# Performance work log

Measured on AMD Instinct MI355X. Metric: run time of the kernel, lower is better.

The kernel has to match this reference:

```python
import jax, jax.numpy as jnp
import numpy as np

N_NODES = 100000
N_EDGES = 1600000
D = 32  # atom and bond feature dim


def _mlp(x, W1, b1, W2, b2, W3, b3):
    # fff: Linear(in,128) -> ReLU -> Linear(128,64) -> ReLU -> Linear(64,32)
    h = jax.nn.relu(x @ W1 + b1)
    h = jax.nn.relu(h @ W2 + b2)
    return h @ W3 + b3


def _init_mlp(key, in_dim):
    ks = jax.random.split(key, 3)
    def lin(k, fan_in, fan_out):
        bound = 1.0 / np.sqrt(fan_in)
        kw, kb = jax.random.split(k)
        W = jax.random.uniform(kw, (fan_in, fan_out), jnp.float32, -bound, bound)
        b = jax.random.uniform(kb, (fan_out,), jnp.float32, -bound, bound)
        return W, b
    W1, b1 = lin(ks[0], in_dim, 128)
    W2, b2 = lin(ks[1], 128, 64)
    W3, b3 = lin(ks[2], 64, 32)
    return W1, b1, W2, b2, W3, b3


def setup_inputs() -> dict:
    key = jax.random.key(0)
    k_bonds, k_a1, k_a2, k_atoms, k_e, k_v = jax.random.split(key, 6)
    inp = {
        "bonds": jax.random.normal(k_bonds, (N_EDGES, D), jnp.float32),
        "bond_atom_1": jax.random.randint(k_a1, (N_EDGES,), 0, N_NODES, jnp.int64),
        "bond_atom_2": jax.random.randint(k_a2, (N_EDGES,), 0, N_NODES, jnp.int64),
        "atoms": jax.random.normal(k_atoms, (N_NODES, D), jnp.float32),
    }
    We1, be1, We2, be2, We3, be3 = _init_mlp(k_e, 96)
    Wv1, bv1, Wv2, bv2, Wv3, bv3 = _init_mlp(k_v, 64)
    inp.update(We1=We1, be1=be1, We2=We2, be2=be2, We3=We3, be3=be3,
               Wv1=Wv1, bv1=bv1, Wv2=Wv2, bv2=bv2, Wv3=Wv3, bv3=bv3)
    return inp


def reference(bonds, bond_atom_1, bond_atom_2, atoms,
              We1, be1, We2, be2, We3, be3,
              Wv1, bv1, Wv2, bv2, Wv3, bv3):
    # Edge update: gather endpoint atom features, concat with bond feats, MLP
    atom1 = atoms[bond_atom_1]                    # [E, D]
    atom2 = atoms[bond_atom_2]                    # [E, D]
    e_in = jnp.concatenate([atom1, atom2, bonds], axis=1)  # [E, 3D]
    new_bonds = _mlp(e_in, We1, be1, We2, be2, We3, be3)    # [E, 32]

    # Node update: scatter-mean new bond features onto target atoms
    # (PyG default flow aggregates messages at edge_index[1] == bond_atom_2)
    n = atoms.shape[0]
    seg_sum = jax.ops.segment_sum(new_bonds, bond_atom_2, num_segments=n)
    counts = jax.ops.segment_sum(jnp.ones((new_bonds.shape[0],), new_bonds.dtype),
                                 bond_atom_2, num_segments=n)
    mean_bonds = seg_sum / jnp.maximum(counts, 1.0)[:, None]  # [N, 32]

    v_in = jnp.concatenate([mean_bonds, atoms], axis=1)        # [N, 64]
    new_atoms = _mlp(v_in, Wv1, bv1, Wv2, bv2, Wv3, bv3)       # [N, 32]
    return (new_atoms, new_bonds)
```

## Files before the change

### kernel.cpp

```cpp
#include <hip/hip_runtime.h>
#include <hip/hip_bf16.h>

#define NN 100000
#define NE 1600000
#define NB_SCAN 391

typedef __attribute__((ext_vector_type(8))) short bfrag8;
typedef __attribute__((ext_vector_type(4))) float f32x4;
typedef __attribute__((ext_vector_type(4))) unsigned short us4;
typedef __attribute__((ext_vector_type(8))) unsigned short us8;

__device__ __forceinline__ unsigned short f2bf(float f) {
  unsigned int u = __float_as_uint(f);
  u += 0x7fffu + ((u >> 16) & 1u);
  return (unsigned short)(u >> 16);
}

__device__ __forceinline__ f32x4 mfma16(bfrag8 a, bfrag8 b, f32x4 c) {
  return __builtin_amdgcn_mfma_f32_16x16x32_bf16(a, b, c, 0, 0, 0);
}

__device__ __forceinline__ bfrag8 ld_cvt8(const float* p) {
  float4 a = *(const float4*)p;
  float4 b = *(const float4*)(p + 4);
  bfrag8 r;
  r[0] = (short)f2bf(a.x); r[1] = (short)f2bf(a.y);
  r[2] = (short)f2bf(a.z); r[3] = (short)f2bf(a.w);
  r[4] = (short)f2bf(b.x); r[5] = (short)f2bf(b.y);
  r[6] = (short)f2bf(b.z); r[7] = (short)f2bf(b.w);
  return r;
}

__device__ __forceinline__ void gload_lds16(const void* g, void* l) {
  __builtin_amdgcn_global_load_lds(
      (const __attribute__((address_space(1))) unsigned int*)g,
      (__attribute__((address_space(3))) unsigned int*)l, 16, 0, 0);
}

__device__ __forceinline__ void stage8(unsigned short* dst, const float* src) {
  float4 a = *(const float4*)src;
  float4 b = *(const float4*)(src + 4);
  us8 o;
  o[0] = f2bf(a.x); o[1] = f2bf(a.y); o[2] = f2bf(a.z); o[3] = f2bf(a.w);
  o[4] = f2bf(b.x); o[5] = f2bf(b.y); o[6] = f2bf(b.z); o[7] = f2bf(b.w);
  *(us8*)dst = o;
}

__global__ void pack_w(const float* __restrict__ src, unsigned short* __restrict__ dst,
                       int K, int N) {
  int i = blockIdx.x * 256 + threadIdx.x;
  if (i >= K * N) return;
  int j = i & 7;
  int gc = i >> 3;
  int c = gc % N;
  int g = gc / N;
  dst[i] = f2bf(src[(g * 8 + j) * N + c]);
}

__global__ void count_k(const int* __restrict__ a2, int* __restrict__ cnt) {
  int e = blockIdx.x * 256 + threadIdx.x;
  if (e < NE) atomicAdd(&cnt[a2[e]], 1);
}

__global__ void scan_blocks(const int* __restrict__ cnt, int* __restrict__ off,
                            int* __restrict__ bsum) {
  __shared__ int s[256];
  const int t = threadIdx.x;
  const int idx = blockIdx.x * 256 + t;
  int v = (idx < NN) ? cnt[idx] : 0;
  s[t] = v;
  __syncthreads();
  for (int d = 1; d < 256; d <<= 1) {
    int x = (t >= d) ? s[t - d] : 0;
    __syncthreads();
    s[t] += x;
    __syncthreads();
  }
  if (idx < NN) off[idx] = s[t] - v;
  if (t == 255) bsum[blockIdx.x] = s[255];
}

__global__ void scan_bsum(int* __restrict__ bsum) {
  __shared__ int s[512];
  const int t = threadIdx.x;
  int v = (t < NB_SCAN) ? bsum[t] : 0;
  s[t] = v;
  __syncthreads();
  for (int d = 1; d < 512; d <<= 1) {
    int x = (t >= d) ? s[t - d] : 0;
    __syncthreads();
    s[t] += x;
    __syncthreads();
  }
  if (t < NB_SCAN) bsum[t] = s[t] - v;
}

__global__ void scan_finalize(int* __restrict__ off, const int* __restrict__ bsum,
                              int* __restrict__ cursor) {
  int idx = blockIdx.x * 256 + threadIdx.x;
  if (idx < NN) {
    int o = off[idx] + bsum[blockIdx.x];
    off[idx] = o;
    cursor[idx] = o;
  }
  if (idx == 0) off[NN] = NE;
}

__global__ void fill_csr(const int* __restrict__ a2, int* __restrict__ cursor,
                         int* __restrict__ csr) {
  int e = blockIdx.x * 256 + threadIdx.x;
  if (e < NE) {
    int p = atomicAdd(&cursor[a2[e]], 1);
    csr[p] = e;
  }
}

__global__ __launch_bounds__(256, 2) void edge_kernel(
    const float* __restrict__ bonds, const int* __restrict__ a1p, const int* __restrict__ a2p,
    const float* __restrict__ atoms,
    const float* __restrict__ be1, const float* __restrict__ be2, const float* __restrict__ be3,
    const unsigned short* __restrict__ wpack,
    float* __restrict__ new_bonds) {
  __shared__ unsigned short sW[22528];
  __shared__ float sB1[128], sB2[64], sB3[32];
  __shared__ unsigned short sH1[128 * 136];

  const int tid = threadIdx.x;
  const int lane = tid & 63, wv = tid >> 6;
  const int cl = lane & 15, q = lane >> 4;
  const int e0 = blockIdx.x * 128;

  {
    const char* src = (const char*)wpack;
    char* dst = (char*)sW;
#pragma unroll
    for (int i = 0; i < 11; ++i) {
      const int c = i * 4 + wv;
      gload_lds16(src + c * 1024 + lane * 16, dst + c * 1024);
    }
  }
  if (tid < 128) sB1[tid] = be1[tid];
  else if (tid < 192) sB2[tid - 128] = be2[tid - 128];
  else if (tid < 224) sB3[tid - 192] = be3[tid - 192];

  bfrag8 xb[2][3];
#pragma unroll
  for (int t = 0; t < 2; ++t) {
    const int e = e0 + wv * 32 + t * 16 + cl;
    const int ia1 = a1p[e];
    const int ia2 = a2p[e];
    xb[t][0] = ld_cvt8(atoms + (size_t)ia1 * 32 + q * 8);
    xb[t][1] = ld_cvt8(atoms + (size_t)ia2 * 32 + q * 8);
    xb[t][2] = ld_cvt8(bonds + (size_t)e * 32 + q * 8);
  }
  __syncthreads();

#pragma unroll
  for (int rt = 0; rt < 8; ++rt) {
    const unsigned short* wa = &sW[(q * 128 + rt * 16 + cl) * 8];
    bfrag8 w0 = *(const bfrag8*)(wa);
    bfrag8 w1 = *(const bfrag8*)(wa + 4096);
    bfrag8 w2 = *(const bfrag8*)(wa + 8192);
    f32x4 acc[2];
    acc[0] = (f32x4){0.f, 0.f, 0.f, 0.f};
    acc[1] = (f32x4){0.f, 0.f, 0.f, 0.f};
#pragma unroll
    for (int t = 0; t < 2; ++t) {
      acc[t] = mfma16(w0, xb[t][0], acc[t]);
      acc[t] = mfma16(w1, xb[t][1], acc[t]);
      acc[t] = mfma16(w2, xb[t][2], acc[t]);
    }
    const int c0 = rt * 16 + q * 4;
#pragma unroll
    for (int t = 0; t < 2; ++t) {
      us4 hv;
#pragma unroll
      for (int r = 0; r < 4; ++r) hv[r] = f2bf(fmaxf(acc[t][r] + sB1[c0 + r], 0.f));
      *(us4*)&sH1[(wv * 32 + t * 16 + cl) * 136 + c0] = hv;
    }
  }
  __syncthreads();

  bfrag8 hb[4][2];
#pragma unroll
  for (int t = 0; t < 2; ++t) {
    const unsigned short* hr = &sH1[(wv * 32 + t * 16 + cl) * 136 + q * 8];
#pragma unroll
    for (int ks = 0; ks < 4; ++ks) hb[ks][t] = *(const bfrag8*)(hr + ks * 32);
  }
  __syncthreads();

  unsigned short* sH2 = sH1;
#pragma unroll
  for (int rt = 0; rt < 4; ++rt) {
    f32x4 acc[2];
    acc[0] = (f32x4){0.f, 0.f, 0.f, 0.f};
    acc[1] = (f32x4){0.f, 0.f, 0.f, 0.f};
#pragma unroll
    for (int ks = 0; ks < 4; ++ks) {
      bfrag8 w = *(const bfrag8*)&sW[12288 + ks * 2048 + (q * 64 + rt * 16 + cl) * 8];
#pragma unroll
      for (int t = 0; t < 2; ++t) acc[t] = mfma16(w, hb[ks][t], acc[t]);
    }
    const int c0 = rt * 16 + q * 4;
#pragma unroll
    for (int t = 0; t < 2; ++t) {
      us4 hv;
#pragma unroll
      for (int r = 0; r < 4; ++r) hv[r] = f2bf(fmaxf(acc[t][r] + sB2[c0 + r], 0.f));
      *(us4*)&sH2[(wv * 32 + t * 16 + cl) * 72 + c0] = hv;
    }
  }
  __syncthreads();

  bfrag8 gb0[2], gb1[2];
#pragma unroll
  for (int t = 0; t < 2; ++t) {
    const unsigned short* hr = &sH2[(wv * 32 + t * 16 + cl) * 72 + q * 8];
    gb0[t] = *(const bfrag8*)(hr);
    gb1[t] = *(const bfrag8*)(hr + 32);
  }
#pragma unroll
  for (int rt = 0; rt < 2; ++rt) {
    bfrag8 w0 = *(const bfrag8*)&sW[20480 + (q * 32 + rt * 16 + cl) * 8];
    bfrag8 w1 = *(const bfrag8*)&sW[20480 + 1024 + (q * 32 + rt * 16 + cl) * 8];
    const int c0 = rt * 16 + q * 4;
#pragma unroll
    for (int t = 0; t < 2; ++t) {
      f32x4 acc = {0.f, 0.f, 0.f, 0.f};
      acc = mfma16(w0, gb0[t], acc);
      acc = mfma16(w1, gb1[t], acc);
      const int e = e0 + wv * 32 + t * 16 + cl;
      float4 o;
      o.x = acc[0] + sB3[c0 + 0];
      o.y = acc[1] + sB3[c0 + 1];
      o.z = acc[2] + sB3[c0 + 2];
      o.w = acc[3] + sB3[c0 + 3];
      *(float4*)(new_bonds + (size_t)e * 32 + c0) = o;
    }
  }
}

__global__ __launch_bounds__(256, 2) void node_kernel(
    const float* __restrict__ atoms,
    const float* __restrict__ bv1, const float* __restrict__ bv2, const float* __restrict__ bv3,
    const unsigned short* __restrict__ wpack,
    const int* __restrict__ off, const int* __restrict__ csr,
    const float* __restrict__ new_bonds, float* __restrict__ new_atoms) {
  __shared__ unsigned short sW[18432];
  __shared__ float sB1[128], sB2[64], sB3[32];
  __shared__ unsigned short sV[64 * 72];
  __shared__ unsigned short sH1[64 * 136];

  const int tid = threadIdx.x;
  const int lane = tid & 63, wv = tid >> 6;
  const int n0 = blockIdx.x * 64;

  {
    const uint4* src = (const uint4*)wpack;
    uint4* dst = (uint4*)sW;
#pragma unroll
    for (int i = 0; i < 9; ++i) dst[tid + i * 256] = src[tid + i * 256];
  }
  if (tid < 128) sB1[tid] = bv1[tid];
  if (tid < 64) sB2[tid] = bv2[tid];
  if (tid < 32) sB3[tid] = bv3[tid];

  {
    const int nl = tid >> 2, l4 = tid & 3;
    const int n = n0 + nl;
    unsigned short* vd = &sV[nl * 72 + l4 * 8];
    if (n < NN) {
      const int o0 = off[n], o1 = off[n + 1];
      float s0x = 0.f, s0y = 0.f, s0z = 0.f, s0w = 0.f;
      float s1x = 0.f, s1y = 0.f, s1z = 0.f, s1w = 0.f;
      int i = o0;
      if (i < o1) {
        int e = csr[i];
        while (++i < o1) {
          int en = csr[i];
          const float4* r = (const float4*)(new_bonds + (size_t)e * 32 + l4 * 8);
          float4 a = r[0], b = r[1];
          s0x += a.x; s0y += a.y; s0z += a.z; s0w += a.w;
          s1x += b.x; s1y += b.y; s1z += b.z; s1w += b.w;
          e = en;
        }
        const float4* r = (const float4*)(new_bonds + (size_t)e * 32 + l4 * 8);
        float4 a = r[0], b = r[1];
        s0x += a.x; s0y += a.y; s0z += a.z; s0w += a.w;
        s1x += b.x; s1y += b.y; s1z += b.z; s1w += b.w;
      }
      const float inv = 1.0f / fmaxf((float)(o1 - o0), 1.0f);
      us8 m;
      m[0] = f2bf(s0x * inv); m[1] = f2bf(s0y * inv);
      m[2] = f2bf(s0z * inv); m[3] = f2bf(s0w * inv);
      m[4] = f2bf(s1x * inv); m[5] = f2bf(s1y * inv);
      m[6] = f2bf(s1z * inv); m[7] = f2bf(s1w * inv);
      *(us8*)vd = m;
      stage8(&sV[nl * 72 + 32 + l4 * 8], atoms + (size_t)n * 32 + l4 * 8);
    } else {
      us8 z = {0, 0, 0, 0, 0, 0, 0, 0};
      *(us8*)vd = z;
      *(us8*)&sV[nl * 72 + 32 + l4 * 8] = z;
    }
  }
  __syncthreads();

  const int cl = lane & 15, q = lane >> 4;
  const int nt = wv * 16;
  const int ng = n0 + nt + cl;

  bfrag8 vb0 = *(const bfrag8*)&sV[(nt + cl) * 72 + q * 8];
  bfrag8 vb1 = *(const bfrag8*)&sV[(nt + cl) * 72 + 32 + q * 8];
#pragma unroll
  for (int rt = 0; rt < 8; ++rt) {
    f32x4 acc = {0.f, 0.f, 0.f, 0.f};
    acc = mfma16(*(const bfrag8*)&sW[(q * 128 + rt * 16 + cl) * 8], vb0, acc);
    acc = mfma16(*(const bfrag8*)&sW[4096 + (q * 128 + rt * 16 + cl) * 8], vb1, acc);
    const int c0 = rt * 16 + q * 4;
    us4 hv;
#pragma unroll
    for (int r = 0; r < 4; ++r) {
      float v = acc[r] + sB1[c0 + r];
      hv[r] = f2bf(fmaxf(v, 0.f));
    }
    *(us4*)&sH1[(nt + cl) * 136 + c0] = hv;
  }
  __syncthreads();

  bfrag8 hb[4];
  {
    const unsigned short* hr = &sH1[(nt + cl) * 136 + q * 8];
#pragma unroll
    for (int ks = 0; ks < 4; ++ks) hb[ks] = *(const bfrag8*)(hr + ks * 32);
  }
#pragma unroll
  for (int rt = 0; rt < 4; ++rt) {
    f32x4 acc = {0.f, 0.f, 0.f, 0.f};
#pragma unroll
    for (int ks = 0; ks < 4; ++ks)
      acc = mfma16(*(const bfrag8*)&sW[8192 + ks * 2048 + (q * 64 + rt * 16 + cl) * 8], hb[ks], acc);
    const int c0 = rt * 16 + q * 4;
    us4 hv;
#pragma unroll
    for (int r = 0; r < 4; ++r) {
      float v = acc[r] + sB2[c0 + r];
      hv[r] = f2bf(fmaxf(v, 0.f));
    }
    *(us4*)&sV[(nt + cl) * 72 + c0] = hv;
  }
  __syncthreads();

  bfrag8 gb0 = *(const bfrag8*)&sV[(nt + cl) * 72 + q * 8];
  bfrag8 gb1 = *(const bfrag8*)&sV[(nt + cl) * 72 + 32 + q * 8];
  if (ng < NN) {
    float* outp = new_atoms + (size_t)ng * 32;
#pragma unroll
    for (int rt = 0; rt < 2; ++rt) {
      f32x4 acc = {0.f, 0.f, 0.f, 0.f};
      acc = mfma16(*(const bfrag8*)&sW[16384 + (q * 32 + rt * 16 + cl) * 8], gb0, acc);
      acc = mfma16(*(const bfrag8*)&sW[16384 + 1024 + (q * 32 + rt * 16 + cl) * 8], gb1, acc);
      const int c0 = rt * 16 + q * 4;
      float4 o;
      o.x = acc[0] + sB3[c0 + 0];
      o.y = acc[1] + sB3[c0 + 1];
      o.z = acc[2] + sB3[c0 + 2];
      o.w = acc[3] + sB3[c0 + 3];
      *(float4*)(outp + c0) = o;
    }
  }
}

extern "C" void kernel_launch(void* const* d_in, const int* in_sizes, int n_in,
                              void* d_out, int out_size, void* d_ws, size_t ws_size,
                              hipStream_t stream) {
  const float* bonds = (const float*)d_in[0];
  const int* a1 = (const int*)d_in[1];
  const int* a2 = (const int*)d_in[2];
  const float* atoms = (const float*)d_in[3];
  const float* We1 = (const float*)d_in[4];
  const float* be1 = (const float*)d_in[5];
  const float* We2 = (const float*)d_in[6];
  const float* be2 = (const float*)d_in[7];
  const float* We3 = (const float*)d_in[8];
  const float* be3 = (const float*)d_in[9];
  const float* Wv1 = (const float*)d_in[10];
  const float* bv1 = (const float*)d_in[11];
  const float* Wv2 = (const float*)d_in[12];
  const float* bv2 = (const float*)d_in[13];
  const float* Wv3 = (const float*)d_in[14];
  const float* bv3 = (const float*)d_in[15];

  float* out = (float*)d_out;
  float* new_atoms = out;
  float* new_bonds = out + (size_t)NN * 32;

  char* ws = (char*)d_ws;
  int* cnt    = (int*)(ws + 0);
  int* off    = (int*)(ws + 400000);
  int* cursor = (int*)(ws + 800016);
  int* bsum   = (int*)(ws + 1200064);
  unsigned short* wp = (unsigned short*)(ws + 1202176);
  int* csr    = (int*)(ws + 1284096);

  hipMemsetAsync(cnt, 0, (size_t)NN * 4, stream);

  pack_w<<<48, 256, 0, stream>>>(We1, wp + 0, 96, 128);
  pack_w<<<32, 256, 0, stream>>>(We2, wp + 12288, 128, 64);
  pack_w<<<8, 256, 0, stream>>>(We3, wp + 20480, 64, 32);
  pack_w<<<32, 256, 0, stream>>>(Wv1, wp + 22528, 64, 128);
  pack_w<<<32, 256, 0, stream>>>(Wv2, wp + 30720, 128, 64);
  pack_w<<<8, 256, 0, stream>>>(Wv3, wp + 38912, 64, 32);

  count_k<<<(NE + 255) / 256, 256, 0, stream>>>(a2, cnt);
  scan_blocks<<<NB_SCAN, 256, 0, stream>>>(cnt, off, bsum);
  scan_bsum<<<1, 512, 0, stream>>>(bsum);
  scan_finalize<<<NB_SCAN, 256, 0, stream>>>(off, bsum, cursor);
  fill_csr<<<(NE + 255) / 256, 256, 0, stream>>>(a2, cursor, csr);

  edge_kernel<<<NE / 128, 256, 0, stream>>>(bonds, a1, a2, atoms, be1, be2, be3, wp,
                                            new_bonds);
  node_kernel<<<(NN + 63) / 64, 256, 0, stream>>>(atoms, bv1, bv2, bv3, wp + 22528,
                                                  off, csr, new_bonds, new_atoms);
}
```

Baseline: 456.4 us.

## Persistent edge/node kernels with prefetch, bf16 atom table, and packed bf16 conversion

Edge and node kernels become persistent grid-stride loops over fixed 512-block grids. The edge kernel register-prefetches the next tile's gathered inputs and the index after that, so load latency overlaps the MFMA work, and weights are staged into LDS once per block. A pre-pass converts atoms to a bf16 table, halving gather bytes and removing per-edge conversion. Scalar bf16 rounding is replaced by the v_cvt_pk_bf16_f32 instruction, the node aggregation is unrolled by two, and the cursor buffer is reused. The cost is an extra conversion kernel and higher register pressure.

```diff
diff --git a/kernel.cpp b/kernel.cpp
--- a/kernel.cpp
+++ b/kernel.cpp
@@ -4,11 +4,14 @@
 #define NN 100000
 #define NE 1600000
 #define NB_SCAN 391
+#define ETILES 12500
+#define EGRID 512
+#define NGRID 512
 
 typedef __attribute__((ext_vector_type(8))) short bfrag8;
 typedef __attribute__((ext_vector_type(4))) float f32x4;
-typedef __attribute__((ext_vector_type(4))) unsigned short us4;
 typedef __attribute__((ext_vector_type(8))) unsigned short us8;
+typedef __attribute__((ext_vector_type(4))) unsigned int u32x4;
 
 __device__ __forceinline__ unsigned short f2bf(float f) {
   unsigned int u = __float_as_uint(f);
@@ -16,19 +19,31 @@
   return (unsigned short)(u >> 16);
 }
 
+__device__ __forceinline__ unsigned int pk2(float a, float b) {
+  unsigned int r;
+  asm("v_cvt_pk_bf16_f32 %0, %1, %2" : "=v"(r) : "v"(a), "v"(b));
+  return r;
+}
+
+__device__ __forceinline__ uint2 pk4(float v0, float v1, float v2, float v3) {
+  return make_uint2(pk2(v0, v1), pk2(v2, v3));
+}
+
+__device__ __forceinline__ bfrag8 pack8(float4 a, float4 b) {
+  union { u32x4 u; bfrag8 f; } c;
+  c.u[0] = pk2(a.x, a.y); c.u[1] = pk2(a.z, a.w);
+  c.u[2] = pk2(b.x, b.y); c.u[3] = pk2(b.z, b.w);
+  return c.f;
+}
+
+__device__ __forceinline__ bfrag8 as_frag(us8 v) {
+  union { us8 u; bfrag8 f; } c;
+  c.u = v;
+  return c.f;
+}
+
 __device__ __forceinline__ f32x4 mfma16(bfrag8 a, bfrag8 b, f32x4 c) {
   return __builtin_amdgcn_mfma_f32_16x16x32_bf16(a, b, c, 0, 0, 0);
-}
-
-__device__ __forceinline__ bfrag8 ld_cvt8(const float* p) {
-  float4 a = *(const float4*)p;
-  float4 b = *(const float4*)(p + 4);
-  bfrag8 r;
-  r[0] = (short)f2bf(a.x); r[1] = (short)f2bf(a.y);
-  r[2] = (short)f2bf(a.z); r[3] = (short)f2bf(a.w);
-  r[4] = (short)f2bf(b.x); r[5] = (short)f2bf(b.y);
-  r[6] = (short)f2bf(b.z); r[7] = (short)f2bf(b.w);
-  return r;
 }
 
 __device__ __forceinline__ void gload_lds16(const void* g, void* l) {
@@ -37,13 +52,10 @@
       (__attribute__((address_space(3))) unsigned int*)l, 16, 0, 0);
 }
 
-__device__ __forceinline__ void stage8(unsigned short* dst, const float* src) {
-  float4 a = *(const float4*)src;
-  float4 b = *(const float4*)(src + 4);
-  us8 o;
-  o[0] = f2bf(a.x); o[1] = f2bf(a.y); o[2] = f2bf(a.z); o[3] = f2bf(a.w);
-  o[4] = f2bf(b.x); o[5] = f2bf(b.y); o[6] = f2bf(b.z); o[7] = f2bf(b.w);
-  *(us8*)dst = o;
+__global__ void cvt_atoms(const float* __restrict__ src, unsigned short* __restrict__ dst) {
+  int i = blockIdx.x * 256 + threadIdx.x;
+  float4 v = *(const float4*)(src + (size_t)i * 4);
+  *(uint2*)(dst + (size_t)i * 4) = pk4(v.x, v.y, v.z, v.w);
 }
 
 __global__ void pack_w(const float* __restrict__ src, unsigned short* __restrict__ dst,
@@ -117,7 +129,7 @@
 
 __global__ __launch_bounds__(256, 2) void edge_kernel(
     const float* __restrict__ bonds, const int* __restrict__ a1p, const int* __restrict__ a2p,
-    const float* __restrict__ atoms,
+    const unsigned short* __restrict__ atoms_bf,
     const float* __restrict__ be1, const float* __restrict__ be2, const float* __restrict__ be3,
     const unsigned short* __restrict__ wpack,
     float* __restrict__ new_bonds) {
@@ -128,7 +140,7 @@
   const int tid = threadIdx.x;
   const int lane = tid & 63, wv = tid >> 6;
   const int cl = lane & 15, q = lane >> 4;
-  const int e0 = blockIdx.x * 128;
+  const int esub = wv * 32 + cl;
 
   {
     const char* src = (const char*)wpack;
@@ -143,106 +155,150 @@
   else if (tid < 192) sB2[tid - 128] = be2[tid - 128];
   else if (tid < 224) sB3[tid - 192] = be3[tid - 192];
 
-  bfrag8 xb[2][3];
+  int tile = blockIdx.x;
+  us8 ra1[2], ra2[2];
+  float4 rb[2][2];
+  int ia1n[2], ia2n[2];
+
 #pragma unroll
   for (int t = 0; t < 2; ++t) {
-    const int e = e0 + wv * 32 + t * 16 + cl;
-    const int ia1 = a1p[e];
-    const int ia2 = a2p[e];
-    xb[t][0] = ld_cvt8(atoms + (size_t)ia1 * 32 + q * 8);
-    xb[t][1] = ld_cvt8(atoms + (size_t)ia2 * 32 + q * 8);
-    xb[t][2] = ld_cvt8(bonds + (size_t)e * 32 + q * 8);
+    const int e = tile * 128 + esub + t * 16;
+    const int ia1 = a1p[e], ia2 = a2p[e];
+    ra1[t] = *(const us8*)(atoms_bf + (size_t)ia1 * 32 + q * 8);
+    ra2[t] = *(const us8*)(atoms_bf + (size_t)ia2 * 32 + q * 8);
+    const float* bp = bonds + (size_t)e * 32 + q * 8;
+    rb[t][0] = *(const float4*)(bp);
+    rb[t][1] = *(const float4*)(bp + 4);
+  }
+  {
+    int tn = tile + EGRID; if (tn >= ETILES) tn = tile;
+#pragma unroll
+    for (int t = 0; t < 2; ++t) {
+      const int e = tn * 128 + esub + t * 16;
+      ia1n[t] = a1p[e]; ia2n[t] = a2p[e];
+    }
   }
   __syncthreads();
 
-#pragma unroll
-  for (int rt = 0; rt < 8; ++rt) {
-    const unsigned short* wa = &sW[(q * 128 + rt * 16 + cl) * 8];
-    bfrag8 w0 = *(const bfrag8*)(wa);
-    bfrag8 w1 = *(const bfrag8*)(wa + 4096);
-    bfrag8 w2 = *(const bfrag8*)(wa + 8192);
-    f32x4 acc[2];
-    acc[0] = (f32x4){0.f, 0.f, 0.f, 0.f};
-    acc[1] = (f32x4){0.f, 0.f, 0.f, 0.f};
+  for (; tile < ETILES; tile += EGRID) {
+    bfrag8 xb0[2], xb1[2], xb2[2];
 #pragma unroll
     for (int t = 0; t < 2; ++t) {
-      acc[t] = mfma16(w0, xb[t][0], acc[t]);
-      acc[t] = mfma16(w1, xb[t][1], acc[t]);
-      acc[t] = mfma16(w2, xb[t][2], acc[t]);
-    }
-    const int c0 = rt * 16 + q * 4;
+      xb0[t] = as_frag(ra1[t]);
+      xb1[t] = as_frag(ra2[t]);
+      xb2[t] = pack8(rb[t][0], rb[t][1]);
+    }
+    const int tn = (tile + EGRID < ETILES) ? tile + EGRID : tile;
 #pragma unroll
     for (int t = 0; t < 2; ++t) {
-      us4 hv;
-#pragma unroll
-      for (int r = 0; r < 4; ++r) hv[r] = f2bf(fmaxf(acc[t][r] + sB1[c0 + r], 0.f));
-      *(us4*)&sH1[(wv * 32 + t * 16 + cl) * 136 + c0] = hv;
-    }
-  }
-  __syncthreads();
-
-  bfrag8 hb[4][2];
-#pragma unroll
-  for (int t = 0; t < 2; ++t) {
-    const unsigned short* hr = &sH1[(wv * 32 + t * 16 + cl) * 136 + q * 8];
-#pragma unroll
-    for (int ks = 0; ks < 4; ++ks) hb[ks][t] = *(const bfrag8*)(hr + ks * 32);
-  }
-  __syncthreads();
-
-  unsigned short* sH2 = sH1;
-#pragma unroll
-  for (int rt = 0; rt < 4; ++rt) {
-    f32x4 acc[2];
-    acc[0] = (f32x4){0.f, 0.f, 0.f, 0.f};
-    acc[1] = (f32x4){0.f, 0.f, 0.f, 0.f};
-#pragma unroll
-    for (int ks = 0; ks < 4; ++ks) {
-      bfrag8 w = *(const bfrag8*)&sW[12288 + ks * 2048 + (q * 64 + rt * 16 + cl) * 8];
-#pragma unroll
-      for (int t = 0; t < 2; ++t) acc[t] = mfma16(w, hb[ks][t], acc[t]);
-    }
-    const int c0 = rt * 16 + q * 4;
+      ra1[t] = *(const us8*)(atoms_bf + (size_t)ia1n[t] * 32 + q * 8);
+      ra2[t] = *(const us8*)(atoms_bf + (size_t)ia2n[t] * 32 + q * 8);
+      const int e = tn * 128 + esub + t * 16;
+      const float* bp = bonds + (size_t)e * 32 + q * 8;
+      rb[t][0] = *(const float4*)(bp);
+      rb[t][1] = *(const float4*)(bp + 4);
+    }
+    {
+      int tnn = tile + 2 * EGRID; if (tnn >= ETILES) tnn = tn;
+#pragma unroll
+      for (int t = 0; t < 2; ++t) {
+        const int e = tnn * 128 + esub + t * 16;
+        ia1n[t] = a1p[e]; ia2n[t] = a2p[e];
+      }
+    }
+
+#pragma unroll
+    for (int rt = 0; rt < 8; ++rt) {
+      const unsigned short* wa = &sW[(q * 128 + rt * 16 + cl) * 8];
+      bfrag8 w0 = *(const bfrag8*)(wa);
+      bfrag8 w1 = *(const bfrag8*)(wa + 4096);
+      bfrag8 w2 = *(const bfrag8*)(wa + 8192);
+      f32x4 acc[2];
+      acc[0] = (f32x4){0.f, 0.f, 0.f, 0.f};
+      acc[1] = (f32x4){0.f, 0.f, 0.f, 0.f};
+#pragma unroll
+      for (int t = 0; t < 2; ++t) {
+        acc[t] = mfma16(w0, xb0[t], acc[t]);
+        acc[t] = mfma16(w1, xb1[t], acc[t]);
+        acc[t] = mfma16(w2, xb2[t], acc[t]);
+      }
+      const int c0 = rt * 16 + q * 4;
+#pragma unroll
+      for (int t = 0; t < 2; ++t) {
+        uint2 hv = pk4(fmaxf(acc[t][0] + sB1[c0 + 0], 0.f),
+                       fmaxf(acc[t][1] + sB1[c0 + 1], 0.f),
+                       fmaxf(acc[t][2] + sB1[c0 + 2], 0.f),
+                       fmaxf(acc[t][3] + sB1[c0 + 3], 0.f));
+        *(uint2*)&sH1[(esub + t * 16) * 136 + c0] = hv;
+      }
+    }
+    __syncthreads();
+
+    bfrag8 hb[4][2];
 #pragma unroll
     for (int t = 0; t < 2; ++t) {
-      us4 hv;
-#pragma unroll
-      for (int r = 0; r < 4; ++r) hv[r] = f2bf(fmaxf(acc[t][r] + sB2[c0 + r], 0.f));
-      *(us4*)&sH2[(wv * 32 + t * 16 + cl) * 72 + c0] = hv;
-    }
-  }
-  __syncthreads();
-
-  bfrag8 gb0[2], gb1[2];
-#pragma unroll
-  for (int t = 0; t < 2; ++t) {
-    const unsigned short* hr = &sH2[(wv * 32 + t * 16 + cl) * 72 + q * 8];
-    gb0[t] = *(const bfrag8*)(hr);
-    gb1[t] = *(const bfrag8*)(hr + 32);
-  }
-#pragma unroll
-  for (int rt = 0; rt < 2; ++rt) {
-    bfrag8 w0 = *(const bfrag8*)&sW[20480 + (q * 32 + rt * 16 + cl) * 8];
-    bfrag8 w1 = *(const bfrag8*)&sW[20480 + 1024 + (q * 32 + rt * 16 + cl) * 8];
-    const int c0 = rt * 16 + q * 4;
+      const unsigned short* hr = &sH1[(esub + t * 16) * 136 + q * 8];
+#pragma unroll
+      for (int ks = 0; ks < 4; ++ks) hb[ks][t] = *(const bfrag8*)(hr + ks * 32);
+    }
+    __syncthreads();
+
+    unsigned short* sH2 = sH1;
+#pragma unroll
+    for (int rt = 0; rt < 4; ++rt) {
+      f32x4 acc[2];
+      acc[0] = (f32x4){0.f, 0.f, 0.f, 0.f};
+      acc[1] = (f32x4){0.f, 0.f, 0.f, 0.f};
+#pragma unroll
+      for (int ks = 0; ks < 4; ++ks) {
+        bfrag8 w = *(const bfrag8*)&sW[12288 + ks * 2048 + (q * 64 + rt * 16 + cl) * 8];
+#pragma unroll
+        for (int t = 0; t < 2; ++t) acc[t] = mfma16(w, hb[ks][t], acc[t]);
+      }
+      const int c0 = rt * 16 + q * 4;
+#pragma unroll
+      for (int t = 0; t < 2; ++t) {
+        uint2 hv = pk4(fmaxf(acc[t][0] + sB2[c0 + 0], 0.f),
+                       fmaxf(acc[t][1] + sB2[c0 + 1], 0.f),
+                       fmaxf(acc[t][2] + sB2[c0 + 2], 0.f),
+                       fmaxf(acc[t][3] + sB2[c0 + 3], 0.f));
+        *(uint2*)&sH2[(esub + t * 16) * 72 + c0] = hv;
+      }
+    }
+    __syncthreads();
+
+    bfrag8 gb0[2], gb1[2];
 #pragma unroll
     for (int t = 0; t < 2; ++t) {
-      f32x4 acc = {0.f, 0.f, 0.f, 0.f};
-      acc = mfma16(w0, gb0[t], acc);
-      acc = mfma16(w1, gb1[t], acc);
-      const int e = e0 + wv * 32 + t * 16 + cl;
-      float4 o;
-      o.x = acc[0] + sB3[c0 + 0];
-      o.y = acc[1] + sB3[c0 + 1];
-      o.z = acc[2] + sB3[c0 + 2];
-      o.w = acc[3] + sB3[c0 + 3];
-      *(float4*)(new_bonds + (size_t)e * 32 + c0) = o;
-    }
+      const unsigned short* hr = &sH2[(esub + t * 16) * 72 + q * 8];
+      gb0[t] = *(const bfrag8*)(hr);
+      gb1[t] = *(const bfrag8*)(hr + 32);
+    }
+#pragma unroll
+    for (int rt = 0; rt < 2; ++rt) {
+      bfrag8 w0 = *(const bfrag8*)&sW[20480 + (q * 32 + rt * 16 + cl) * 8];
+      bfrag8 w1 = *(const bfrag8*)&sW[20480 + 1024 + (q * 32 + rt * 16 + cl) * 8];
+      const int c0 = rt * 16 + q * 4;
+#pragma unroll
+      for (int t = 0; t < 2; ++t) {
+        f32x4 acc = {0.f, 0.f, 0.f, 0.f};
+        acc = mfma16(w0, gb0[t], acc);
+        acc = mfma16(w1, gb1[t], acc);
+        const int e = tile * 128 + esub + t * 16;
+        float4 o;
+        o.x = acc[0] + sB3[c0 + 0];
+        o.y = acc[1] + sB3[c0 + 1];
+        o.z = acc[2] + sB3[c0 + 2];
+        o.w = acc[3] + sB3[c0 + 3];
+        *(float4*)(new_bonds + (size_t)e * 32 + c0) = o;
+      }
+    }
+    __syncthreads();
   }
 }
 
 __global__ __launch_bounds__(256, 2) void node_kernel(
-    const float* __restrict__ atoms,
+    const unsigned short* __restrict__ atoms_bf,
     const float* __restrict__ bv1, const float* __restrict__ bv2, const float* __restrict__ bv3,
     const unsigned short* __restrict__ wpack,
     const int* __restrict__ off, const int* __restrict__ csr,
@@ -254,7 +310,8 @@
 
   const int tid = threadIdx.x;
   const int lane = tid & 63, wv = tid >> 6;
-  const int n0 = blockIdx.x * 64;
+  const int cl = lane & 15, q = lane >> 4;
+  const int nl = tid >> 2, l4 = tid & 3;
 
   {
     const uint4* src = (const uint4*)wpack;
@@ -266,107 +323,110 @@
   if (tid < 64) sB2[tid] = bv2[tid];
   if (tid < 32) sB3[tid] = bv3[tid];
 
-  {
-    const int nl = tid >> 2, l4 = tid & 3;
-    const int n = n0 + nl;
-    unsigned short* vd = &sV[nl * 72 + l4 * 8];
-    if (n < NN) {
-      const int o0 = off[n], o1 = off[n + 1];
-      float s0x = 0.f, s0y = 0.f, s0z = 0.f, s0w = 0.f;
-      float s1x = 0.f, s1y = 0.f, s1z = 0.f, s1w = 0.f;
-      int i = o0;
-      if (i < o1) {
-        int e = csr[i];
-        while (++i < o1) {
-          int en = csr[i];
-          const float4* r = (const float4*)(new_bonds + (size_t)e * 32 + l4 * 8);
-          float4 a = r[0], b = r[1];
-          s0x += a.x; s0y += a.y; s0z += a.z; s0w += a.w;
-          s1x += b.x; s1y += b.y; s1z += b.z; s1w += b.w;
-          e = en;
+  for (int n0 = blockIdx.x * 64; n0 < NN; n0 += NGRID * 64) {
+    __syncthreads();
+
+    {
+      const int n = n0 + nl;
+      unsigned short* vd = &sV[nl * 72 + l4 * 8];
+      if (n < NN) {
+        const int o0 = off[n], o1 = off[n + 1];
+        float4 sa0 = {0.f, 0.f, 0.f, 0.f}, sa1 = {0.f, 0.f, 0.f, 0.f};
+        float4 sb0 = {0.f, 0.f, 0.f, 0.f}, sb1 = {0.f, 0.f, 0.f, 0.f};
+        int i = o0;
+        for (; i + 1 < o1; i += 2) {
+          const int ea = csr[i], eb = csr[i + 1];
+          const float4* pa = (const float4*)(new_bonds + (size_t)ea * 32 + l4 * 8);
+          const float4* pb = (const float4*)(new_bonds + (size_t)eb * 32 + l4 * 8);
+          float4 a0 = pa[0], a1 = pa[1];
+          float4 b0 = pb[0], b1 = pb[1];
+          sa0.x += a0.x; sa0.y += a0.y; sa0.z += a0.z; sa0.w += a0.w;
+          sa1.x += a1.x; sa1.y += a1.y; sa1.z += a1.z; sa1.w += a1.w;
+          sb0.x += b0.x; sb0.y += b0.y; sb0.z += b0.z; sb0.w += b0.w;
+          sb1.x += b1.x; sb1.y += b1.y; sb1.z += b1.z; sb1.w += b1.w;
         }
-        const float4* r = (const float4*)(new_bonds + (size_t)e * 32 + l4 * 8);
-        float4 a = r[0], b = r[1];
-        s0x += a.x; s0y += a.y; s0z += a.z; s0w += a.w;
-        s1x += b.x; s1y += b.y; s1z += b.z; s1w += b.w;
-      }
-      const float inv = 1.0f / fmaxf((float)(o1 - o0), 1.0f);
-      us8 m;
-      m[0] = f2bf(s0x * inv); m[1] = f2bf(s0y * inv);
-      m[2] = f2bf(s0z * inv); m[3] = f2bf(s0w * inv);
-      m[4] = f2bf(s1x * inv); m[5] = f2bf(s1y * inv);
-      m[6] = f2bf(s1z * inv); m[7] = f2bf(s1w * inv);
-      *(us8*)vd = m;
-      stage8(&sV[nl * 72 + 32 + l4 * 8], atoms + (size_t)n * 32 + l4 * 8);
-    } else {
-      us8 z = {0, 0, 0, 0, 0, 0, 0, 0};
-      *(us8*)vd = z;
-      *(us8*)&sV[nl * 72 + 32 + l4 * 8] = z;
-    }
-  }
-  __syncthreads();
-
-  const int cl = lane & 15, q = lane >> 4;
-  const int nt = wv * 16;
-  const int ng = n0 + nt + cl;
-
-  bfrag8 vb0 = *(const bfrag8*)&sV[(nt + cl) * 72 + q * 8];
-  bfrag8 vb1 = *(const bfrag8*)&sV[(nt + cl) * 72 + 32 + q * 8];
-#pragma unroll
-  for (int rt = 0; rt < 8; ++rt) {
-    f32x4 acc = {0.f, 0.f, 0.f, 0.f};
-    acc = mfma16(*(const bfrag8*)&sW[(q * 128 + rt * 16 + cl) * 8], vb0, acc);
-    acc = mfma16(*(const bfrag8*)&sW[4096 + (q * 128 + rt * 16 + cl) * 8], vb1, acc);
-    const int c0 = rt * 16 + q * 4;
-    us4 hv;
-#pragma unroll
-    for (int r = 0; r < 4; ++r) {
-      float v = acc[r] + sB1[c0 + r];
-      hv[r] = f2bf(fmaxf(v, 0.f));
-    }
-    *(us4*)&sH1[(nt + cl) * 136 + c0] = hv;
-  }
-  __syncthreads();
-
-  bfrag8 hb[4];
-  {
-    const unsigned short* hr = &sH1[(nt + cl) * 136 + q * 8];
-#pragma unroll
-    for (int ks = 0; ks < 4; ++ks) hb[ks] = *(const bfrag8*)(hr + ks * 32);
-  }
-#pragma unroll
-  for (int rt = 0; rt < 4; ++rt) {
-    f32x4 acc = {0.f, 0.f, 0.f, 0.f};
-#pragma unroll
-    for (int ks = 0; ks < 4; ++ks)
-      acc = mfma16(*(const bfrag8*)&sW[8192 + ks * 2048 + (q * 64 + rt * 16 + cl) * 8], hb[ks], acc);
-    const int c0 = rt * 16 + q * 4;
-    us4 hv;
-#pragma unroll
-    for (int r = 0; r < 4; ++r) {
-      float v = acc[r] + sB2[c0 + r];
-      hv[r] = f2bf(fmaxf(v, 0.f));
-    }
-    *(us4*)&sV[(nt + cl) * 72 + c0] = hv;
-  }
-  __syncthreads();
-
-  bfrag8 gb0 = *(const bfrag8*)&sV[(nt + cl) * 72 + q * 8];
-  bfrag8 gb1 = *(const bfrag8*)&sV[(nt + cl) * 72 + 32 + q * 8];
-  if (ng < NN) {
-    float* outp = new_atoms + (size_t)ng * 32;
-#pragma unroll
-    for (int rt = 0; rt < 2; ++rt) {
+        if (i < o1) {
+          const int ea = csr[i];
+          const float4* pa = (const float4*)(new_bonds + (size_t)ea * 32 + l4 * 8);
+          float4 a0 = pa[0], a1 = pa[1];
+          sa0.x += a0.x; sa0.y += a0.y; sa0.z += a0.z; sa0.w += a0.w;
+          sa1.x += a1.x; sa1.y += a1.y; sa1.z += a1.z; sa1.w += a1.w;
+        }
+        const float inv = 1.0f / fmaxf((float)(o1 - o0), 1.0f);
+        uint4 m;
+        m.x = pk2((sa0.x + sb0.x) * inv, (sa0.y + sb0.y) * inv);
+        m.y = pk2((sa0.z + sb0.z) * inv, (sa0.w + sb0.w) * inv);
+        m.z = pk2((sa1.x + sb1.x) * inv, (sa1.y + sb1.y) * inv);
+        m.w = pk2((sa1.z + sb1.z) * inv, (sa1.w + sb1.w) * inv);
+        *(uint4*)vd = m;
+        *(us8*)&sV[nl * 72 + 32 + l4 * 8] =
+            *(const us8*)(atoms_bf + (size_t)n * 32 + l4 * 8);
+      } else {
+        us8 z = {0, 0, 0, 0, 0, 0, 0, 0};
+        *(us8*)vd = z;
+        *(us8*)&sV[nl * 72 + 32 + l4 * 8] = z;
+      }
+    }
+    __syncthreads();
+
+    const int nt = wv * 16;
+    const int ng = n0 + nt + cl;
+
+    bfrag8 vb0 = *(const bfrag8*)&sV[(nt + cl) * 72 + q * 8];
+    bfrag8 vb1 = *(const bfrag8*)&sV[(nt + cl) * 72 + 32 + q * 8];
+#pragma unroll
+    for (int rt = 0; rt < 8; ++rt) {
       f32x4 acc = {0.f, 0.f, 0.f, 0.f};
-      acc = mfma16(*(const bfrag8*)&sW[16384 + (q * 32 + rt * 16 + cl) * 8], gb0, acc);
-      acc = mfma16(*(const bfrag8*)&sW[16384 + 1024 + (q * 32 + rt * 16 + cl) * 8], gb1, acc);
+      acc = mfma16(*(const bfrag8*)&sW[(q * 128 + rt * 16 + cl) * 8], vb0, acc);
+      acc = mfma16(*(const bfrag8*)&sW[4096 + (q * 128 + rt * 16 + cl) * 8], vb1, acc);
       const int c0 = rt * 16 + q * 4;
-      float4 o;
-      o.x = acc[0] + sB3[c0 + 0];
-      o.y = acc[1] + sB3[c0 + 1];
-      o.z = acc[2] + sB3[c0 + 2];
-      o.w = acc[3] + sB3[c0 + 3];
-      *(float4*)(outp + c0) = o;
+      uint2 hv = pk4(fmaxf(acc[0] + sB1[c0 + 0], 0.f),
+                     fmaxf(acc[1] + sB1[c0 + 1], 0.f),
+                     fmaxf(acc[2] + sB1[c0 + 2], 0.f),
+                     fmaxf(acc[3] + sB1[c0 + 3], 0.f));
+      *(uint2*)&sH1[(nt + cl) * 136 + c0] = hv;
+    }
+    __syncthreads();
+
+    bfrag8 hb[4];
+    {
+      const unsigned short* hr = &sH1[(nt + cl) * 136 + q * 8];
+#pragma unroll
+      for (int ks = 0; ks < 4; ++ks) hb[ks] = *(const bfrag8*)(hr + ks * 32);
+    }
+    __syncthreads();
+#pragma unroll
+    for (int rt = 0; rt < 4; ++rt) {
+      f32x4 acc = {0.f, 0.f, 0.f, 0.f};
+#pragma unroll
+      for (int ks = 0; ks < 4; ++ks)
+        acc = mfma16(*(const bfrag8*)&sW[8192 + ks * 2048 + (q * 64 + rt * 16 + cl) * 8], hb[ks], acc);
+      const int c0 = rt * 16 + q * 4;
+      uint2 hv = pk4(fmaxf(acc[0] + sB2[c0 + 0], 0.f),
+                     fmaxf(acc[1] + sB2[c0 + 1], 0.f),
+                     fmaxf(acc[2] + sB2[c0 + 2], 0.f),
+                     fmaxf(acc[3] + sB2[c0 + 3], 0.f));
+      *(uint2*)&sV[(nt + cl) * 72 + c0] = hv;
+    }
+    __syncthreads();
+
+    bfrag8 gb0 = *(const bfrag8*)&sV[(nt + cl) * 72 + q * 8];
+    bfrag8 gb1 = *(const bfrag8*)&sV[(nt + cl) * 72 + 32 + q * 8];
+    if (ng < NN) {
+      float* outp = new_atoms + (size_t)ng * 32;
+#pragma unroll
+      for (int rt = 0; rt < 2; ++rt) {
+        f32x4 acc = {0.f, 0.f, 0.f, 0.f};
+        acc = mfma16(*(const bfrag8*)&sW[16384 + (q * 32 + rt * 16 + cl) * 8], gb0, acc);
+        acc = mfma16(*(const bfrag8*)&sW[16384 + 1024 + (q * 32 + rt * 16 + cl) * 8], gb1, acc);
+        const int c0 = rt * 16 + q * 4;
+        float4 o;
+        o.x = acc[0] + sB3[c0 + 0];
+        o.y = acc[1] + sB3[c0 + 1];
+        o.z = acc[2] + sB3[c0 + 2];
+        o.w = acc[3] + sB3[c0 + 3];
+        *(float4*)(outp + c0) = o;
+      }
     }
   }
 }
@@ -398,12 +458,14 @@
   char* ws = (char*)d_ws;
   int* cnt    = (int*)(ws + 0);
   int* off    = (int*)(ws + 400000);
-  int* cursor = (int*)(ws + 800016);
-  int* bsum   = (int*)(ws + 1200064);
-  unsigned short* wp = (unsigned short*)(ws + 1202176);
-  int* csr    = (int*)(ws + 1284096);
+  int* bsum   = (int*)(ws + 800016);
+  unsigned short* wp = (unsigned short*)(ws + 802064);
+  int* csr    = (int*)(ws + 883984);
+  unsigned short* atoms_bf = (unsigned short*)(ws + 7283984);
 
   hipMemsetAsync(cnt, 0, (size_t)NN * 4, stream);
+
+  cvt_atoms<<<3125, 256, 0, stream>>>(atoms, atoms_bf);
 
   pack_w<<<48, 256, 0, stream>>>(We1, wp + 0, 96, 128);
   pack_w<<<32, 256, 0, stream>>>(We2, wp + 12288, 128, 64);
@@ -415,11 +477,11 @@
   count_k<<<(NE + 255) / 256, 256, 0, stream>>>(a2, cnt);
   scan_blocks<<<NB_SCAN, 256, 0, stream>>>(cnt, off, bsum);
   scan_bsum<<<1, 512, 0, stream>>>(bsum);
-  scan_finalize<<<NB_SCAN, 256, 0, stream>>>(off, bsum, cursor);
-  fill_csr<<<(NE + 255) / 256, 256, 0, stream>>>(a2, cursor, csr);
-
-  edge_kernel<<<NE / 128, 256, 0, stream>>>(bonds, a1, a2, atoms, be1, be2, be3, wp,
-                                            new_bonds);
-  node_kernel<<<(NN + 63) / 64, 256, 0, stream>>>(atoms, bv1, bv2, bv3, wp + 22528,
-                                                  off, csr, new_bonds, new_atoms);
-}
+  scan_finalize<<<NB_SCAN, 256, 0, stream>>>(off, bsum, cnt);
+  fill_csr<<<(NE + 255) / 256, 256, 0, stream>>>(a2, cnt, csr);
+
+  edge_kernel<<<EGRID, 256, 0, stream>>>(bonds, a1, a2, atoms_bf, be1, be2, be3, wp,
+                                         new_bonds);
+  node_kernel<<<NGRID, 256, 0, stream>>>(atoms_bf, bv1, bv2, bv3, wp + 22528,
+                                         off, csr, new_bonds, new_atoms);
+}
```

After: 437.2 us. -4.2%, faster.
